# Optimization experiments

Hardware: AMD Instinct MI355X
Metric: run time of the kernel (lower is better)

The kernel has to match this reference:

```python
import jax, jax.numpy as jnp
import numpy as np

N_NODES = 20000
N_EDGES = 160000
DIM = 64          # node embedding dim
SUB = 16          # sub_dim
NB = 5            # n_bonds_type
RB = 8            # radial basis size (FeNNol default)
CUTOFF = 5.0
NLAYERS = 3
HID = 64          # conv_hidden
NSPEC = 86        # species onehot size
XI_SHAPE = RB * SUB * NB   # 640
FC_IN = XI_SHAPE + SUB     # 656
LOG2 = float(np.log(2.0))


def ssp(x):
    # shifted softplus activation
    return jax.nn.softplus(x) - jnp.asarray(LOG2, x.dtype)


def radial_bessel(r):
    # sine Bessel radial basis on [0, cutoff]; r: [E] -> [E, RB]
    n = jnp.arange(1, RB + 1, dtype=r.dtype)
    x = r[:, None]
    return jnp.sqrt(jnp.asarray(2.0 / CUTOFF, r.dtype)) * jnp.sin(n * jnp.pi * x / CUTOFF) / x


def setup_inputs() -> dict:
    key = jax.random.key(0)
    ks = jax.random.split(key, 16)
    inp = {}
    inp['species'] = jax.random.randint(ks[0], (N_NODES,), 1, NSPEC, dtype=jnp.int32)
    inp['edge_src'] = jnp.sort(jax.random.randint(ks[1], (N_EDGES,), 0, N_NODES, dtype=jnp.int32))
    inp['edge_dst'] = jax.random.randint(ks[2], (N_EDGES,), 0, N_NODES, dtype=jnp.int32)
    # distances kept away from 0 to keep 1/r finite
    inp['distances'] = jax.random.uniform(ks[3], (N_EDGES,), jnp.float32, 0.5, CUTOFF)
    inp['switch'] = jax.random.uniform(ks[4], (N_EDGES,), jnp.float32)
    inp['bond_order'] = jax.random.uniform(ks[5], (N_EDGES, NB), jnp.float32)
    s = lambda fan: 1.0 / np.sqrt(fan)
    inp['W_species'] = jax.random.normal(ks[6], (NSPEC, DIM), jnp.float32) * s(NSPEC)
    inp['Wl'] = jax.random.normal(ks[7], (NLAYERS, DIM, 2 * SUB), jnp.float32) * s(DIM)
    inp['bl'] = jnp.zeros((NLAYERS, 2 * SUB), jnp.float32)
    inp['fcW1'] = jax.random.normal(ks[8], (NLAYERS, FC_IN, HID), jnp.float32) * s(FC_IN)
    inp['fcb1'] = jnp.zeros((NLAYERS, HID), jnp.float32)
    inp['fcW2'] = jax.random.normal(ks[9], (NLAYERS, HID, HID), jnp.float32) * s(HID)
    inp['fcb2'] = jnp.zeros((NLAYERS, HID), jnp.float32)
    inp['fcW3'] = jax.random.normal(ks[10], (NLAYERS, HID, DIM), jnp.float32) * s(HID)
    inp['fcb3'] = jnp.zeros((NLAYERS, DIM), jnp.float32)
    return inp


def reference(species, edge_src, edge_dst, distances, switch, bond_order,
              W_species, Wl, bl, fcW1, fcb1, fcW2, fcb2, fcW3, fcb3):
    # onehot(species) @ W (no bias) == embedding gather
    xi = W_species[species]                      # [N, DIM]
    rb = radial_bessel(distances)                # [E, RB]
    sw = switch[:, None]                         # [E, 1]
    for l in range(NLAYERS):
        h = xi @ Wl[l] + bl[l]                   # [N, 2*SUB]
        si, mi = h[:, :SUB], h[:, SUB:]
        # per-edge outer product: [E, RB, SUB, NB] -> [E, RB*SUB*NB]
        xi_j = (rb[:, :, None, None]
                * mi[edge_dst][:, None, :, None]
                * bond_order[:, None, None, :]).reshape(N_EDGES, XI_SHAPE)
        dxi = jax.ops.segment_sum(xi_j * sw, edge_src, num_segments=N_NODES)  # [N, 640]
        dxi = jnp.concatenate([dxi, si], axis=-1)                             # [N, 656]
        dxi = ssp(dxi @ fcW1[l] + fcb1[l])
        dxi = ssp(dxi @ fcW2[l] + fcb2[l])
        dxi = dxi @ fcW3[l] + fcb3[l]            # last FC layer linear
        xi = xi + dxi
    return xi
```

## Files before the change

kernel.cpp:

```cpp
#include <hip/hip_runtime.h>
#include <math.h>

#define N_NODES 20000
#define N_EDGES 160000
#define EPAD    160256
#define NGROUPS (EPAD / 8)
#define GSTRIDE 320
#define NTILES  1250

#define PI_F 3.14159265358979323846f
#define LN2_F 0.69314718055994530942f

#define W1PK 43008
#define W23PK 4096
#define WPK_LAYER 51200
#define WLPK_LAYER 2048
#define XROW 680
#define CAP 312
#define NFILL_MAX 272

#define NW_EDGE 626
#define NW_XI   625
#define NW_PACK 616
#define NW_ROW  79
#define NW_TOTAL (NW_EDGE + NW_XI + NW_PACK + NW_ROW)

typedef short short8v __attribute__((ext_vector_type(8)));
typedef float f32x4 __attribute__((ext_vector_type(4)));
typedef unsigned short u16;
typedef unsigned long long ull;

__device__ __forceinline__ float sspf(float x) {
    return fmaxf(x, 0.0f) + log1pf(expf(-fabsf(x))) - LN2_F;
}
__device__ __forceinline__ u16 f2bf(float f) {
    unsigned int u = __float_as_uint(f);
    return (u16)((u + 0x7fffu + ((u >> 16) & 1u)) >> 16);
}
__device__ __forceinline__ unsigned int pk2(float a, float b) {
    return (unsigned int)f2bf(a) | ((unsigned int)f2bf(b) << 16);
}
__device__ __forceinline__ ull mge(int t) {
    t = t < 0 ? 0 : (t > 4 ? 4 : t);
    return t == 4 ? 0ULL : (~0ULL << (t * 16));
}

__device__ void edge_wt_work(int blk, const float* __restrict__ dist,
                             const float* __restrict__ sw,
                             const float* __restrict__ bo,
                             u16* __restrict__ WTg, char* smem)
{
    u16 (*tr)[264] = reinterpret_cast<u16(*)[264]>(smem);
    int tid = threadIdx.x;
    int e = blk * 256 + tid;

    if (e < N_EDGES) {
        float r = dist[e];
        float c = sqrtf(0.4f) / r * sw[e];
        float th = PI_F * r * 0.2f;
        float s1, c1;
        __sincosf(th, &s1, &c1);
        float k2c = 2.0f * c1;
        float rbv[8];
        rbv[0] = s1;
        float sp = 0.0f, sc = s1;
        #pragma unroll
        for (int n = 1; n < 8; ++n) {
            float sn = k2c * sc - sp;
            rbv[n] = sn;
            sp = sc; sc = sn;
        }
        #pragma unroll
        for (int n = 0; n < 8; ++n) rbv[n] *= c;
        float bov[5];
        #pragma unroll
        for (int b = 0; b < 5; ++b) bov[b] = bo[(size_t)e * 5 + b];
        #pragma unroll
        for (int n = 0; n < 8; ++n)
            #pragma unroll
            for (int b = 0; b < 5; ++b)
                tr[n * 5 + b][tid] = f2bf(rbv[n] * bov[b]);
    } else {
        #pragma unroll
        for (int j = 0; j < 40; ++j) tr[j][tid] = 0;
    }
    __syncthreads();

    #pragma unroll
    for (int i = 0; i < 5; ++i) {
        int r = i * 8 + (tid & 7);
        int gl = tid >> 3;
        uint4 v = *reinterpret_cast<const uint4*>(&tr[r][gl * 8]);
        *reinterpret_cast<uint4*>(
            WTg + ((size_t)(blk * 32 + gl) * GSTRIDE + r * 8)) = v;
    }
}

__device__ void row_start_work(int blk, const int* __restrict__ src,
                               int* __restrict__ row)
{
    int i = blk * 256 + threadIdx.x;
    if (i > N_NODES) return;
    int lo = 0, hi = N_EDGES;
    while (lo < hi) {
        int mid = (lo + hi) >> 1;
        if (src[mid] < i) lo = mid + 1; else hi = mid;
    }
    row[i] = lo;
}

__device__ void pack_w_work(int blk, const float* __restrict__ fcW1,
                            const float* __restrict__ fcW2,
                            const float* __restrict__ fcW3,
                            const float* __restrict__ Wl,
                            u16* __restrict__ Wpk,
                            u16* __restrict__ Wlpk)
{
    int idx = blk * 256 + threadIdx.x;
    if (idx >= 3 * WPK_LAYER + 2 * WLPK_LAYER) return;
    if (idx >= 3 * WPK_LAYER) {
        int r2 = idx - 3 * WPK_LAYER;
        int layer2 = r2 >> 11;
        int e = r2 & 2047;
        int j = e & 7, lane = (e >> 3) & 63;
        int rest = e >> 9;
        int ks = rest >> 1, cf = rest & 1;
        int k = ks * 32 + (lane >> 4) * 8 + j;
        int col = cf * 16 + (lane & 15);
        Wlpk[(size_t)layer2 * WLPK_LAYER + e] =
            f2bf(Wl[(size_t)(layer2 + 1) * 64 * 32 + (size_t)k * 32 + col]);
        return;
    }
    int layer = idx / WPK_LAYER;
    int r = idx - layer * WPK_LAYER;
    float val = 0.0f;
    if (r < W1PK) {
        int e = r;
        int j = e & 7, lane = (e >> 3) & 63, c16 = (e >> 9) & 3, ks = e >> 11;
        int k = ks * 32 + (lane >> 4) * 8 + j;
        int colm = c16 * 16 + (lane & 15);
        if (k < 640) {
            int nbv = k >> 4, ss = k & 15;
            int nn = nbv / 5, bb = nbv - nn * 5;
            val = fcW1[(size_t)layer * 656 * 64 + (size_t)(nn * 80 + ss * 5 + bb) * 64 + colm];
        } else if (k < 656) {
            val = fcW1[(size_t)layer * 656 * 64 + (size_t)k * 64 + colm];
        }
    } else {
        bool is2 = (r < W1PK + W23PK);
        const float* W = is2 ? fcW2 : fcW3;
        int e = is2 ? (r - W1PK) : (r - W1PK - W23PK);
        int j = e & 7, lane = (e >> 3) & 63, c16 = (e >> 9) & 3, ks = e >> 11;
        int k = ks * 32 + (lane >> 4) * 8 + j;
        int colm = c16 * 16 + (lane & 15);
        val = W[(size_t)layer * 64 * 64 + (size_t)k * 64 + colm];
    }
    Wpk[(size_t)layer * WPK_LAYER + r] = f2bf(val);
}

__device__ void xi_init_h_work(int blk, const int* __restrict__ species,
                               const float* __restrict__ Wsp,
                               const float* __restrict__ Wl0,
                               const float* __restrict__ bl0,
                               float* __restrict__ xi,
                               float* __restrict__ h, char* smem)
{
    float* xs = reinterpret_cast<float*>(smem);
    float* ws = reinterpret_cast<float*>(smem + 8192);
    int tid = threadIdx.x;
    int nb = blk * 32;

    #pragma unroll
    for (int i = 0; i < 2; ++i) {
        int idx = tid + i * 256;
        int node = idx >> 4, c4 = idx & 15;
        int sp = species[nb + node];
        float4 v = reinterpret_cast<const float4*>(Wsp + (size_t)sp * 64)[c4];
        reinterpret_cast<float4*>(xs)[idx] = v;
        reinterpret_cast<float4*>(xi)[(size_t)(nb + node) * 16 + c4] = v;
    }
    {
        const float4* wsrc = reinterpret_cast<const float4*>(Wl0);
        float4* wd = reinterpret_cast<float4*>(ws);
        #pragma unroll
        for (int i = 0; i < 2; ++i) wd[tid + i * 256] = wsrc[tid + i * 256];
    }
    __syncthreads();

    int c4g = tid & 7;
    int nrow = tid >> 3;
    float4 acc = *reinterpret_cast<const float4*>(bl0 + c4g * 4);
    const float* xr = xs + nrow * 64;
    #pragma unroll 8
    for (int j = 0; j < 64; ++j) {
        float xv = xr[j];
        float4 wv = *reinterpret_cast<const float4*>(ws + j * 32 + c4g * 4);
        acc.x = fmaf(xv, wv.x, acc.x);
        acc.y = fmaf(xv, wv.y, acc.y);
        acc.z = fmaf(xv, wv.z, acc.z);
        acc.w = fmaf(xv, wv.w, acc.w);
    }
    *reinterpret_cast<float4*>(h + (size_t)(nb + nrow) * 32 + c4g * 4) = acc;
}

__global__ __launch_bounds__(256) void setup_kernel(
    const float* __restrict__ dist, const float* __restrict__ sw,
    const float* __restrict__ bo, u16* __restrict__ WTg,
    const int* __restrict__ species, const float* __restrict__ Wsp,
    const float* __restrict__ Wl, const float* __restrict__ bl0,
    float* __restrict__ xi, float* __restrict__ h0,
    const float* __restrict__ fcW1, const float* __restrict__ fcW2,
    const float* __restrict__ fcW3, u16* __restrict__ Wpk,
    u16* __restrict__ Wlpk,
    const int* __restrict__ esrc, int* __restrict__ rowp)
{
    __shared__ __align__(16) char smem[21760];
    int wk = blockIdx.x;
    if (wk < NW_EDGE)
        edge_wt_work(wk, dist, sw, bo, WTg, smem);
    else if (wk < NW_EDGE + NW_XI)
        xi_init_h_work(wk - NW_EDGE, species, Wsp, Wl, bl0, xi, h0, smem);
    else if (wk < NW_EDGE + NW_XI + NW_PACK)
        pack_w_work(wk - NW_EDGE - NW_XI, fcW1, fcW2, fcW3, Wl, Wpk, Wlpk);
    else
        row_start_work(wk - NW_EDGE - NW_XI - NW_PACK, esrc, rowp);
}

__global__ __launch_bounds__(256) void agg_fc_fused(
    const u16* __restrict__ WTg,
    const int* __restrict__ row,
    const int* __restrict__ dst,
    const float* __restrict__ h_in,
    float* __restrict__ h_out,
    const u16* __restrict__ Wpk,
    const float* __restrict__ b1,
    const float* __restrict__ b2,
    const float* __restrict__ b3,
    const u16* __restrict__ Wlpk_l,
    const float* __restrict__ bl_next,
    int do_h,
    float* __restrict__ xi)
{
    __shared__ __align__(16) char smem[21760 + 16 * CAP * 2];
    u16 (*Xs)[XROW] = reinterpret_cast<u16(*)[XROW]>(smem);
    u16* mi  = reinterpret_cast<u16*>(smem + 21760);
    u16* Y1  = reinterpret_cast<u16*>(smem + 21760);
    u16* Y2  = reinterpret_cast<u16*>(smem + 21760 + 2304);
    float* Yo = reinterpret_cast<float*>(smem + 21760 + 4608);
    u16* Xnb  = reinterpret_cast<u16*>(smem + 8192);

    int tid = threadIdx.x;
    int wv = tid >> 6;
    int lane = tid & 63;
    int s = lane & 15;
    int kg = lane >> 4;
    int n0 = blockIdx.x * 16;
    int base = n0 + (wv << 2);

    int E0 = row[n0];
    int E1 = row[n0 + 16];
    int G0 = E0 & ~7;
    int nfill = E1 - G0;
    if (nfill > NFILL_MAX) nfill = NFILL_MAX;

    {
        int t = kg;
        u16* xr = &Xs[(wv << 2) + t][0];
        xr[640 + s] = f2bf(h_in[(size_t)(base + t) * 32 + s]);
        xr[656 + s] = 0;
    }

    for (int i = tid; i < nfill; i += 256) {
        int d = dst[G0 + i];
        const float4* hp = reinterpret_cast<const float4*>(h_in + (size_t)d * 32 + 16);
        float4 v0 = hp[0], v1 = hp[1], v2 = hp[2], v3 = hp[3];
        u16* col = mi + i;
        col[0 * CAP]  = f2bf(v0.x); col[1 * CAP]  = f2bf(v0.y);
        col[2 * CAP]  = f2bf(v0.z); col[3 * CAP]  = f2bf(v0.w);
        col[4 * CAP]  = f2bf(v1.x); col[5 * CAP]  = f2bf(v1.y);
        col[6 * CAP]  = f2bf(v1.z); col[7 * CAP]  = f2bf(v1.w);
        col[8 * CAP]  = f2bf(v2.x); col[9 * CAP]  = f2bf(v2.y);
        col[10 * CAP] = f2bf(v2.z); col[11 * CAP] = f2bf(v2.w);
        col[12 * CAP] = f2bf(v3.x); col[13 * CAP] = f2bf(v3.y);
        col[14 * CAP] = f2bf(v3.z); col[15 * CAP] = f2bf(v3.w);
    }
    __syncthreads();

    for (int t = 0; t < 4; ++t) {
        int node = base + t;
        int e0 = row[node], e1 = row[node + 1];
        int e0a = e0 & ~7;
        int L0 = e0a - G0;
        int nks = (e1 - e0a + 31) >> 5;

        f32x4 c0 = {0.f, 0.f, 0.f, 0.f};
        f32x4 c1 = {0.f, 0.f, 0.f, 0.f};
        f32x4 c2 = {0.f, 0.f, 0.f, 0.f};

        for (int kc = 0; kc < nks; ++kc) {
            int ebg = e0a + kc * 32 + kg * 8;
            int ebl = L0 + kc * 32 + kg * 8;
            uint4 bu = *reinterpret_cast<const uint4*>(mi + s * CAP + ebl);
            {
                int lo = e0 - ebg, hi = e1 - ebg;
                ull vA = mge(lo) & ~mge(hi);
                ull vB = mge(lo - 4) & ~mge(hi - 4);
                ull* bp = reinterpret_cast<ull*>(&bu);
                bp[0] &= vA;
                bp[1] &= vB;
            }
            short8v bfrag = *reinterpret_cast<short8v*>(&bu);
            const u16* gp = WTg + (size_t)(ebg >> 3) * GSTRIDE + (size_t)s * 8;
            short8v a0 = *reinterpret_cast<const short8v*>(gp);
            short8v a1 = *reinterpret_cast<const short8v*>(gp + 128);
            short8v a2 = {0, 0, 0, 0, 0, 0, 0, 0};
            if (s < 8)
                a2 = *reinterpret_cast<const short8v*>(gp + 256);
            c0 = __builtin_amdgcn_mfma_f32_16x16x32_bf16(a0, bfrag, c0, 0, 0, 0);
            c1 = __builtin_amdgcn_mfma_f32_16x16x32_bf16(a1, bfrag, c1, 0, 0, 0);
            c2 = __builtin_amdgcn_mfma_f32_16x16x32_bf16(a2, bfrag, c2, 0, 0, 0);
        }

        u16* xr = &Xs[(wv << 2) + t][0];
        #pragma unroll
        for (int q = 0; q < 4; ++q) {
            xr[(kg * 4 + q) * 16 + s]      = f2bf(c0[q]);
            xr[(16 + kg * 4 + q) * 16 + s] = f2bf(c1[q]);
        }
        if (kg < 2) {
            #pragma unroll
            for (int q = 0; q < 4; ++q)
                xr[(32 + kg * 4 + q) * 16 + s] = f2bf(c2[q]);
        }
    }
    __syncthreads();

    int w = wv;
    int lrow = lane & 15;
    int lk = lane >> 4;
    int col = w * 16 + lrow;

    const u16* Wpk1 = Wpk;
    const u16* Wpk2 = Wpk + W1PK;
    const u16* Wpk3 = Wpk + W1PK + W23PK;

    f32x4 acc;
    {
        float bv = b1[col];
        acc[0] = bv; acc[1] = bv; acc[2] = bv; acc[3] = bv;
    }
    const u16* wp = Wpk1 + ((size_t)w * 64 + lane) * 8;
    #pragma unroll
    for (int ks = 0; ks < 21; ++ks) {
        short8v a = *reinterpret_cast<const short8v*>(&Xs[lrow][ks * 32 + lk * 8]);
        short8v b = *reinterpret_cast<const short8v*>(wp + (size_t)ks * 2048);
        acc = __builtin_amdgcn_mfma_f32_16x16x32_bf16(a, b, acc, 0, 0, 0);
    }
    __syncthreads();
    #pragma unroll
    for (int q = 0; q < 4; ++q)
        Y1[(lk * 4 + q) * 72 + col] = f2bf(sspf(acc[q]));
    __syncthreads();

    {
        float bv = b2[col];
        acc[0] = bv; acc[1] = bv; acc[2] = bv; acc[3] = bv;
    }
    #pragma unroll
    for (int ks = 0; ks < 2; ++ks) {
        short8v a = *reinterpret_cast<const short8v*>(&Y1[lrow * 72 + ks * 32 + lk * 8]);
        short8v b = *reinterpret_cast<const short8v*>(Wpk2 + ((size_t)(ks * 4 + w) * 64 + lane) * 8);
        acc = __builtin_amdgcn_mfma_f32_16x16x32_bf16(a, b, acc, 0, 0, 0);
    }
    __syncthreads();
    #pragma unroll
    for (int q = 0; q < 4; ++q)
        Y2[(lk * 4 + q) * 72 + col] = f2bf(sspf(acc[q]));
    __syncthreads();

    {
        float bv = b3[col];
        acc[0] = bv; acc[1] = bv; acc[2] = bv; acc[3] = bv;
    }
    #pragma unroll
    for (int ks = 0; ks < 2; ++ks) {
        short8v a = *reinterpret_cast<const short8v*>(&Y2[lrow * 72 + ks * 32 + lk * 8]);
        short8v b = *reinterpret_cast<const short8v*>(Wpk3 + ((size_t)(ks * 4 + w) * 64 + lane) * 8);
        acc = __builtin_amdgcn_mfma_f32_16x16x32_bf16(a, b, acc, 0, 0, 0);
    }
    #pragma unroll
    for (int q = 0; q < 4; ++q)
        Yo[(lk * 4 + q) * 68 + col] = acc[q];
    __syncthreads();

    {
        int rr = tid >> 4;
        int cc = tid & 15;
        float4 dv = *reinterpret_cast<const float4*>(Yo + rr * 68 + cc * 4);
        float4* xpn = reinterpret_cast<float4*>(xi + (size_t)(n0 + rr) * 64 + cc * 4);
        float4 o = *xpn;
        o.x += dv.x; o.y += dv.y; o.z += dv.z; o.w += dv.w;
        *xpn = o;
        if (do_h) {
            unsigned int* xb = reinterpret_cast<unsigned int*>(Xnb + rr * 64 + cc * 4);
            xb[0] = pk2(o.x, o.y);
            xb[1] = pk2(o.z, o.w);
        }
    }

    if (do_h) {
        __syncthreads();
        if (wv < 2) {
            int cf = wv;
            f32x4 hacc;
            {
                float bv = bl_next[cf * 16 + lrow];
                hacc[0] = bv; hacc[1] = bv; hacc[2] = bv; hacc[3] = bv;
            }
            #pragma unroll
            for (int ks = 0; ks < 2; ++ks) {
                short8v a = *reinterpret_cast<const short8v*>(
                    Xnb + lrow * 64 + ks * 32 + lk * 8);
                short8v b = *reinterpret_cast<const short8v*>(
                    Wlpk_l + ((size_t)(ks * 2 + cf) * 64 + lane) * 8);
                hacc = __builtin_amdgcn_mfma_f32_16x16x32_bf16(a, b, hacc, 0, 0, 0);
            }
            #pragma unroll
            for (int q = 0; q < 4; ++q)
                h_out[(size_t)(n0 + lk * 4 + q) * 32 + cf * 16 + lrow] = hacc[q];
        }
    }
}

extern "C" void kernel_launch(void* const* d_in, const int* in_sizes, int n_in,
                              void* d_out, int out_size, void* d_ws, size_t ws_size,
                              hipStream_t stream) {
    const int*   species = (const int*)d_in[0];
    const int*   esrc    = (const int*)d_in[1];
    const int*   edst    = (const int*)d_in[2];
    const float* dist    = (const float*)d_in[3];
    const float* sw      = (const float*)d_in[4];
    const float* bo      = (const float*)d_in[5];
    const float* Wsp     = (const float*)d_in[6];
    const float* Wl      = (const float*)d_in[7];
    const float* bl      = (const float*)d_in[8];
    const float* fcW1    = (const float*)d_in[9];
    const float* fcb1    = (const float*)d_in[10];
    const float* fcW2    = (const float*)d_in[11];
    const float* fcb2    = (const float*)d_in[12];
    const float* fcW3    = (const float*)d_in[13];
    const float* fcb3    = (const float*)d_in[14];
    float* xi = (float*)d_out;

    char* ws = (char*)d_ws;
    u16*   WTg  = (u16*)ws;
    int*   rowp = (int*)(ws + 12820480);
    float* h0   = (float*)(ws + 12900608);
    float* h1   = (float*)(ws + 15460608);
    u16*   Wpk  = (u16*)(ws + 18020608);
    u16*   Wlpk = (u16*)(ws + 18327808);

    hipLaunchKernelGGL(setup_kernel, dim3(NW_TOTAL), dim3(256), 0, stream,
                       dist, sw, bo, WTg,
                       species, Wsp, Wl, bl, xi, h0,
                       fcW1, fcW2, fcW3, Wpk, Wlpk,
                       esrc, rowp);

    float* hbuf[2] = {h0, h1};
    for (int l = 0; l < 3; ++l) {
        int do_h = (l < 2) ? 1 : 0;
        hipLaunchKernelGGL(agg_fc_fused, dim3(NTILES), dim3(256), 0, stream,
                           WTg, rowp, edst,
                           hbuf[l & 1], hbuf[(l + 1) & 1],
                           Wpk + (size_t)l * WPK_LAYER,
                           fcb1 + (size_t)l * 64, fcb2 + (size_t)l * 64,
                           fcb3 + (size_t)l * 64,
                           Wlpk + (size_t)(do_h ? l : 0) * WLPK_LAYER,
                           bl + (size_t)(l + (do_h ? 1 : 0)) * 32,
                           do_h, xi);
    }
}
```

Measured before the change: 84.11 us.

## Recompute edge radial/bond weights in LDS inside fused aggregation kernel

Measured after the change: 84.15 us. No clear change (+0.1%).

```diff
diff --git a/kernel.cpp b/kernel.cpp
--- a/kernel.cpp
+++ b/kernel.cpp
@@ -3,9 +3,6 @@
 
 #define N_NODES 20000
 #define N_EDGES 160000
-#define EPAD    160256
-#define NGROUPS (EPAD / 8)
-#define GSTRIDE 320
 #define NTILES  1250
 
 #define PI_F 3.14159265358979323846f
@@ -16,14 +13,15 @@
 #define WPK_LAYER 51200
 #define WLPK_LAYER 2048
 #define XROW 680
-#define CAP 312
-#define NFILL_MAX 272
-
-#define NW_EDGE 626
+#define CAP 272
+#define NFILL_MAX 232
+#define WT_SLOTS 272
+#define GSTRIDE 320
+
 #define NW_XI   625
 #define NW_PACK 616
 #define NW_ROW  79
-#define NW_TOTAL (NW_EDGE + NW_XI + NW_PACK + NW_ROW)
+#define NW_TOTAL (NW_XI + NW_PACK + NW_ROW)
 
 typedef short short8v __attribute__((ext_vector_type(8)));
 typedef float f32x4 __attribute__((ext_vector_type(4)));
@@ -45,56 +43,6 @@
     return t == 4 ? 0ULL : (~0ULL << (t * 16));
 }
 
-__device__ void edge_wt_work(int blk, const float* __restrict__ dist,
-                             const float* __restrict__ sw,
-                             const float* __restrict__ bo,
-                             u16* __restrict__ WTg, char* smem)
-{
-    u16 (*tr)[264] = reinterpret_cast<u16(*)[264]>(smem);
-    int tid = threadIdx.x;
-    int e = blk * 256 + tid;
-
-    if (e < N_EDGES) {
-        float r = dist[e];
-        float c = sqrtf(0.4f) / r * sw[e];
-        float th = PI_F * r * 0.2f;
-        float s1, c1;
-        __sincosf(th, &s1, &c1);
-        float k2c = 2.0f * c1;
-        float rbv[8];
-        rbv[0] = s1;
-        float sp = 0.0f, sc = s1;
-        #pragma unroll
-        for (int n = 1; n < 8; ++n) {
-            float sn = k2c * sc - sp;
-            rbv[n] = sn;
-            sp = sc; sc = sn;
-        }
-        #pragma unroll
-        for (int n = 0; n < 8; ++n) rbv[n] *= c;
-        float bov[5];
-        #pragma unroll
-        for (int b = 0; b < 5; ++b) bov[b] = bo[(size_t)e * 5 + b];
-        #pragma unroll
-        for (int n = 0; n < 8; ++n)
-            #pragma unroll
-            for (int b = 0; b < 5; ++b)
-                tr[n * 5 + b][tid] = f2bf(rbv[n] * bov[b]);
-    } else {
-        #pragma unroll
-        for (int j = 0; j < 40; ++j) tr[j][tid] = 0;
-    }
-    __syncthreads();
-
-    #pragma unroll
-    for (int i = 0; i < 5; ++i) {
-        int r = i * 8 + (tid & 7);
-        int gl = tid >> 3;
-        uint4 v = *reinterpret_cast<const uint4*>(&tr[r][gl * 8]);
-        *reinterpret_cast<uint4*>(
-            WTg + ((size_t)(blk * 32 + gl) * GSTRIDE + r * 8)) = v;
-    }
-}
 
 __device__ void row_start_work(int blk, const int* __restrict__ src,
                                int* __restrict__ row)
@@ -204,8 +152,6 @@
 }
 
 __global__ __launch_bounds__(256) void setup_kernel(
-    const float* __restrict__ dist, const float* __restrict__ sw,
-    const float* __restrict__ bo, u16* __restrict__ WTg,
     const int* __restrict__ species, const float* __restrict__ Wsp,
     const float* __restrict__ Wl, const float* __restrict__ bl0,
     float* __restrict__ xi, float* __restrict__ h0,
@@ -214,20 +160,20 @@
     u16* __restrict__ Wlpk,
     const int* __restrict__ esrc, int* __restrict__ rowp)
 {
-    __shared__ __align__(16) char smem[21760];
+    __shared__ __align__(16) char smem[16384];
     int wk = blockIdx.x;
-    if (wk < NW_EDGE)
-        edge_wt_work(wk, dist, sw, bo, WTg, smem);
-    else if (wk < NW_EDGE + NW_XI)
-        xi_init_h_work(wk - NW_EDGE, species, Wsp, Wl, bl0, xi, h0, smem);
-    else if (wk < NW_EDGE + NW_XI + NW_PACK)
-        pack_w_work(wk - NW_EDGE - NW_XI, fcW1, fcW2, fcW3, Wl, Wpk, Wlpk);
+    if (wk < NW_XI)
+        xi_init_h_work(wk, species, Wsp, Wl, bl0, xi, h0, smem);
+    else if (wk < NW_XI + NW_PACK)
+        pack_w_work(wk - NW_XI, fcW1, fcW2, fcW3, Wl, Wpk, Wlpk);
     else
-        row_start_work(wk - NW_EDGE - NW_XI - NW_PACK, esrc, rowp);
+        row_start_work(wk - NW_XI - NW_PACK, esrc, rowp);
 }
 
 __global__ __launch_bounds__(256) void agg_fc_fused(
-    const u16* __restrict__ WTg,
+    const float* __restrict__ dist,
+    const float* __restrict__ sw,
+    const float* __restrict__ bo,
     const int* __restrict__ row,
     const int* __restrict__ dst,
     const float* __restrict__ h_in,
@@ -241,9 +187,10 @@
     int do_h,
     float* __restrict__ xi)
 {
-    __shared__ __align__(16) char smem[21760 + 16 * CAP * 2];
+    __shared__ __align__(16) char smem[52224];
     u16 (*Xs)[XROW] = reinterpret_cast<u16(*)[XROW]>(smem);
-    u16* mi  = reinterpret_cast<u16*>(smem + 21760);
+    u16* wt  = reinterpret_cast<u16*>(smem + 21760);
+    u16* mi  = reinterpret_cast<u16*>(smem + 43520);
     u16* Y1  = reinterpret_cast<u16*>(smem + 21760);
     u16* Y2  = reinterpret_cast<u16*>(smem + 21760 + 2304);
     float* Yo = reinterpret_cast<float*>(smem + 21760 + 4608);
@@ -268,6 +215,41 @@
         u16* xr = &Xs[(wv << 2) + t][0];
         xr[640 + s] = f2bf(h_in[(size_t)(base + t) * 32 + s]);
         xr[656 + s] = 0;
+    }
+
+    for (int i = tid; i < WT_SLOTS; i += 256) {
+        int e = G0 + i;
+        u16* wcol = wt + (i >> 3) * GSTRIDE + (i & 7);
+        if (i < nfill && e < N_EDGES) {
+            float r = dist[e];
+            float c = sqrtf(0.4f) / r * sw[e];
+            float th = PI_F * r * 0.2f;
+            float s1, c1v;
+            __sincosf(th, &s1, &c1v);
+            float k2c = 2.0f * c1v;
+            float rbv[8];
+            rbv[0] = s1;
+            float sp = 0.0f, sc = s1;
+            #pragma unroll
+            for (int n = 1; n < 8; ++n) {
+                float sn = k2c * sc - sp;
+                rbv[n] = sn;
+                sp = sc; sc = sn;
+            }
+            #pragma unroll
+            for (int n = 0; n < 8; ++n) rbv[n] *= c;
+            float bov[5];
+            #pragma unroll
+            for (int b = 0; b < 5; ++b) bov[b] = bo[(size_t)e * 5 + b];
+            #pragma unroll
+            for (int n = 0; n < 8; ++n)
+                #pragma unroll
+                for (int b = 0; b < 5; ++b)
+                    wcol[(n * 5 + b) * 8] = f2bf(rbv[n] * bov[b]);
+        } else {
+            #pragma unroll
+            for (int r2 = 0; r2 < 40; ++r2) wcol[r2 * 8] = 0;
+        }
     }
 
     for (int i = tid; i < nfill; i += 256) {
@@ -292,6 +274,8 @@
         int e0a = e0 & ~7;
         int L0 = e0a - G0;
         int nks = (e1 - e0a + 31) >> 5;
+        int maxks = (264 - L0) >> 5;
+        if (nks > maxks) nks = maxks;
 
         f32x4 c0 = {0.f, 0.f, 0.f, 0.f};
         f32x4 c1 = {0.f, 0.f, 0.f, 0.f};
@@ -310,7 +294,7 @@
                 bp[1] &= vB;
             }
             short8v bfrag = *reinterpret_cast<short8v*>(&bu);
-            const u16* gp = WTg + (size_t)(ebg >> 3) * GSTRIDE + (size_t)s * 8;
+            const u16* gp = wt + (ebl >> 3) * GSTRIDE + s * 8;
             short8v a0 = *reinterpret_cast<const short8v*>(gp);
             short8v a1 = *reinterpret_cast<const short8v*>(gp + 128);
             short8v a2 = {0, 0, 0, 0, 0, 0, 0, 0};
@@ -453,15 +437,13 @@
     float* xi = (float*)d_out;
 
     char* ws = (char*)d_ws;
-    u16*   WTg  = (u16*)ws;
-    int*   rowp = (int*)(ws + 12820480);
-    float* h0   = (float*)(ws + 12900608);
-    float* h1   = (float*)(ws + 15460608);
-    u16*   Wpk  = (u16*)(ws + 18020608);
-    u16*   Wlpk = (u16*)(ws + 18327808);
+    int*   rowp = (int*)ws;
+    float* h0   = (float*)(ws + 80128);
+    float* h1   = (float*)(ws + 2640128);
+    u16*   Wpk  = (u16*)(ws + 5200128);
+    u16*   Wlpk = (u16*)(ws + 5507328);
 
     hipLaunchKernelGGL(setup_kernel, dim3(NW_TOTAL), dim3(256), 0, stream,
-                       dist, sw, bo, WTg,
                        species, Wsp, Wl, bl, xi, h0,
                        fcW1, fcW2, fcW3, Wpk, Wlpk,
                        esrc, rowp);
@@ -470,7 +452,7 @@
     for (int l = 0; l < 3; ++l) {
         int do_h = (l < 2) ? 1 : 0;
         hipLaunchKernelGGL(agg_fc_fused, dim3(NTILES), dim3(256), 0, stream,
-                           WTg, rowp, edst,
+                           dist, sw, bo, rowp, edst,
                            hbuf[l & 1], hbuf[(l + 1) & 1],
                            Wpk + (size_t)l * WPK_LAYER,
                            fcb1 + (size_t)l * 64, fcb2 + (size_t)l * 64,
```

## Process two 16-node tiles per block with double-buffered neighbour gather

Applied to the files above, without the earlier changes.

New measurement: 92.65 us. 10.2% more time.

```diff
diff --git a/kernel.cpp b/kernel.cpp
--- a/kernel.cpp
+++ b/kernel.cpp
@@ -6,7 +6,7 @@
 #define EPAD    160256
 #define NGROUPS (EPAD / 8)
 #define GSTRIDE 320
-#define NTILES  1250
+#define NBLK    625
 
 #define PI_F 3.14159265358979323846f
 #define LN2_F 0.69314718055994530942f
@@ -16,8 +16,8 @@
 #define WPK_LAYER 51200
 #define WLPK_LAYER 2048
 #define XROW 680
-#define CAP 312
-#define NFILL_MAX 272
+#define CAP 280
+#define NFILL_MAX 232
 
 #define NW_EDGE 626
 #define NW_XI   625
@@ -241,195 +241,219 @@
     int do_h,
     float* __restrict__ xi)
 {
-    __shared__ __align__(16) char smem[21760 + 16 * CAP * 2];
+    __shared__ __align__(16) char smem[39680];
     u16 (*Xs)[XROW] = reinterpret_cast<u16(*)[XROW]>(smem);
-    u16* mi  = reinterpret_cast<u16*>(smem + 21760);
-    u16* Y1  = reinterpret_cast<u16*>(smem + 21760);
-    u16* Y2  = reinterpret_cast<u16*>(smem + 21760 + 2304);
-    float* Yo = reinterpret_cast<float*>(smem + 21760 + 4608);
-    u16* Xnb  = reinterpret_cast<u16*>(smem + 8192);
+    u16* miA = reinterpret_cast<u16*>(smem + 21760);
+    u16* miB = reinterpret_cast<u16*>(smem + 30720);
+    u16* Xnb = reinterpret_cast<u16*>(smem + 8192);
 
     int tid = threadIdx.x;
     int wv = tid >> 6;
     int lane = tid & 63;
     int s = lane & 15;
     int kg = lane >> 4;
-    int n0 = blockIdx.x * 16;
-    int base = n0 + (wv << 2);
-
-    int E0 = row[n0];
-    int E1 = row[n0 + 16];
-    int G0 = E0 & ~7;
-    int nfill = E1 - G0;
-    if (nfill > NFILL_MAX) nfill = NFILL_MAX;
-
+    int lrow = lane & 15;
+    int lk = lane >> 4;
+    int col = wv * 16 + lrow;
+    int rr = tid >> 4;
+    int cc = tid & 15;
+
+    const u16* Wpk1 = Wpk;
+    const u16* Wpk2 = Wpk + W1PK;
+    const u16* Wpk3 = Wpk + W1PK + W23PK;
+
+    int n0a = blockIdx.x * 32;
+    int n0b = n0a + 16;
+
+    int E0a = row[n0a], E1a = row[n0a + 16];
+    int G0a = E0a & ~7;
+    int nfa = E1a - G0a; if (nfa > NFILL_MAX) nfa = NFILL_MAX;
+    int E0b = row[n0b], E1b = row[n0b + 16];
+    int G0b = E0b & ~7;
+    int nfb = E1b - G0b; if (nfb > NFILL_MAX) nfb = NFILL_MAX;
+
+#define GATHER(G0x, nfx, mix)                                                  \
+    for (int i = tid; i < (nfx); i += 256) {                                   \
+        int d = dst[(G0x) + i];                                                \
+        const float4* hp = reinterpret_cast<const float4*>(h_in + (size_t)d * 32 + 16); \
+        float4 v0 = hp[0], v1 = hp[1], v2 = hp[2], v3 = hp[3];                 \
+        u16* colp = (mix) + i;                                                 \
+        colp[0 * CAP]  = f2bf(v0.x); colp[1 * CAP]  = f2bf(v0.y);              \
+        colp[2 * CAP]  = f2bf(v0.z); colp[3 * CAP]  = f2bf(v0.w);              \
+        colp[4 * CAP]  = f2bf(v1.x); colp[5 * CAP]  = f2bf(v1.y);              \
+        colp[6 * CAP]  = f2bf(v1.z); colp[7 * CAP]  = f2bf(v1.w);              \
+        colp[8 * CAP]  = f2bf(v2.x); colp[9 * CAP]  = f2bf(v2.y);              \
+        colp[10 * CAP] = f2bf(v2.z); colp[11 * CAP] = f2bf(v2.w);              \
+        colp[12 * CAP] = f2bf(v3.x); colp[13 * CAP] = f2bf(v3.y);              \
+        colp[14 * CAP] = f2bf(v3.z); colp[15 * CAP] = f2bf(v3.w);              \
+    }
+
+#define PHASEA(n0x, G0x, mix)                                                  \
+    for (int t = 0; t < 4; ++t) {                                              \
+        int node = (n0x) + (wv << 2) + t;                                      \
+        int e0 = row[node], e1 = row[node + 1];                                \
+        int e0a = e0 & ~7;                                                     \
+        int L0 = e0a - (G0x);                                                  \
+        int nks = (e1 - e0a + 31) >> 5;                                        \
+        int maxks = (272 - L0) >> 5;                                           \
+        if (nks > maxks) nks = maxks;                                          \
+        f32x4 c0 = {0.f, 0.f, 0.f, 0.f};                                       \
+        f32x4 c1 = {0.f, 0.f, 0.f, 0.f};                                       \
+        f32x4 c2 = {0.f, 0.f, 0.f, 0.f};                                       \
+        for (int kc = 0; kc < nks; ++kc) {                                     \
+            int ebg = e0a + kc * 32 + kg * 8;                                  \
+            int ebl = L0 + kc * 32 + kg * 8;                                   \
+            uint4 bu = *reinterpret_cast<const uint4*>((mix) + s * CAP + ebl); \
+            {                                                                  \
+                int lo = e0 - ebg, hi = e1 - ebg;                              \
+                ull vA = mge(lo) & ~mge(hi);                                   \
+                ull vB = mge(lo - 4) & ~mge(hi - 4);                           \
+                ull* bp = reinterpret_cast<ull*>(&bu);                         \
+                bp[0] &= vA;                                                   \
+                bp[1] &= vB;                                                   \
+            }                                                                  \
+            short8v bfrag = *reinterpret_cast<short8v*>(&bu);                  \
+            const u16* gp = WTg + (size_t)(ebg >> 3) * GSTRIDE + (size_t)s * 8;\
+            short8v a0 = *reinterpret_cast<const short8v*>(gp);                \
+            short8v a1 = *reinterpret_cast<const short8v*>(gp + 128);          \
+            short8v a2 = {0, 0, 0, 0, 0, 0, 0, 0};                             \
+            if (s < 8)                                                         \
+                a2 = *reinterpret_cast<const short8v*>(gp + 256);              \
+            c0 = __builtin_amdgcn_mfma_f32_16x16x32_bf16(a0, bfrag, c0, 0, 0, 0); \
+            c1 = __builtin_amdgcn_mfma_f32_16x16x32_bf16(a1, bfrag, c1, 0, 0, 0); \
+            c2 = __builtin_amdgcn_mfma_f32_16x16x32_bf16(a2, bfrag, c2, 0, 0, 0); \
+        }                                                                      \
+        u16* xr = &Xs[(wv << 2) + t][0];                                       \
+        _Pragma("unroll")                                                      \
+        for (int q = 0; q < 4; ++q) {                                          \
+            xr[(kg * 4 + q) * 16 + s]      = f2bf(c0[q]);                      \
+            xr[(16 + kg * 4 + q) * 16 + s] = f2bf(c1[q]);                      \
+        }                                                                      \
+        if (kg < 2) {                                                          \
+            _Pragma("unroll")                                                  \
+            for (int q = 0; q < 4; ++q)                                        \
+                xr[(32 + kg * 4 + q) * 16 + s] = f2bf(c2[q]);                  \
+        }                                                                      \
+    }
+
+#define FC_AND_EPILOGUE(n0x, YREG)                                             \
+    {                                                                          \
+        u16* Y1 = (YREG);                                                      \
+        u16* Y2 = (YREG) + 1152;                        \
+        float* Yo = reinterpret_cast<float*>((YREG) + 2304);   \
+        f32x4 acc;                                                             \
+        {                                                                      \
+            float bv = b1[col];                                                \
+            acc[0] = bv; acc[1] = bv; acc[2] = bv; acc[3] = bv;                \
+        }                                                                      \
+        const u16* wp = Wpk1 + ((size_t)wv * 64 + lane) * 8;                   \
+        _Pragma("unroll")                                                      \
+        for (int ks = 0; ks < 21; ++ks) {                                      \
+            short8v a = *reinterpret_cast<const short8v*>(&Xs[lrow][ks * 32 + lk * 8]); \
+            short8v b = *reinterpret_cast<const short8v*>(wp + (size_t)ks * 2048); \
+            acc = __builtin_amdgcn_mfma_f32_16x16x32_bf16(a, b, acc, 0, 0, 0); \
+        }                                                                      \
+        _Pragma("unroll")                                                      \
+        for (int q = 0; q < 4; ++q)                                            \
+            Y1[(lk * 4 + q) * 72 + col] = f2bf(sspf(acc[q]));                  \
+        __syncthreads();                                                       \
+        {                                                                      \
+            float bv = b2[col];                                                \
+            acc[0] = bv; acc[1] = bv; acc[2] = bv; acc[3] = bv;                \
+        }                                                                      \
+        _Pragma("unroll")                                                      \
+        for (int ks = 0; ks < 2; ++ks) {                                       \
+            short8v a = *reinterpret_cast<const short8v*>(&Y1[lrow * 72 + ks * 32 + lk * 8]); \
+            short8v b = *reinterpret_cast<const short8v*>(Wpk2 + ((size_t)(ks * 4 + wv) * 64 + lane) * 8); \
+            acc = __builtin_amdgcn_mfma_f32_16x16x32_bf16(a, b, acc, 0, 0, 0); \
+        }                                                                      \
+        __syncthreads();                                                       \
+        _Pragma("unroll")                                                      \
+        for (int q = 0; q < 4; ++q)                                            \
+            Y2[(lk * 4 + q) * 72 + col] = f2bf(sspf(acc[q]));                  \
+        __syncthreads();                                                       \
+        {                                                                      \
+            float bv = b3[col];                                                \
+            acc[0] = bv; acc[1] = bv; acc[2] = bv; acc[3] = bv;                \
+        }                                                                      \
+        _Pragma("unroll")                                                      \
+        for (int ks = 0; ks < 2; ++ks) {                                       \
+            short8v a = *reinterpret_cast<const short8v*>(&Y2[lrow * 72 + ks * 32 + lk * 8]); \
+            short8v b = *reinterpret_cast<const short8v*>(Wpk3 + ((size_t)(ks * 4 + wv) * 64 + lane) * 8); \
+            acc = __builtin_amdgcn_mfma_f32_16x16x32_bf16(a, b, acc, 0, 0, 0); \
+        }                                                                      \
+        _Pragma("unroll")                                                      \
+        for (int q = 0; q < 4; ++q)                                            \
+            Yo[(lk * 4 + q) * 68 + col] = acc[q];                              \
+        __syncthreads();                                                       \
+        {                                                                      \
+            float4 dv = *reinterpret_cast<const float4*>(Yo + rr * 68 + cc * 4); \
+            float4* xpn = reinterpret_cast<float4*>(xi + (size_t)((n0x) + rr) * 64 + cc * 4); \
+            float4 o = *xpn;                                                   \
+            o.x += dv.x; o.y += dv.y; o.z += dv.z; o.w += dv.w;                \
+            *xpn = o;                                                          \
+            if (do_h) {                                                        \
+                unsigned int* xb = reinterpret_cast<unsigned int*>(Xnb + rr * 64 + cc * 4); \
+                xb[0] = pk2(o.x, o.y);                                         \
+                xb[1] = pk2(o.z, o.w);                                         \
+            }                                                                  \
+        }                                                                      \
+        if (do_h) {                                                            \
+            __syncthreads();                                                   \
+            if (wv < 2) {                                                      \
+                int cf = wv;                                                   \
+                f32x4 hacc;                                                    \
+                {                                                              \
+                    float bv = bl_next[cf * 16 + lrow];                        \
+                    hacc[0] = bv; hacc[1] = bv; hacc[2] = bv; hacc[3] = bv;    \
+                }                                                              \
+                _Pragma("unroll")                                              \
+                for (int ks = 0; ks < 2; ++ks) {                               \
+                    short8v a = *reinterpret_cast<const short8v*>(             \
+                        Xnb + lrow * 64 + ks * 32 + lk * 8);                   \
+                    short8v b = *reinterpret_cast<const short8v*>(             \
+                        Wlpk_l + ((size_t)(ks * 2 + cf) * 64 + lane) * 8);     \
+                    hacc = __builtin_amdgcn_mfma_f32_16x16x32_bf16(a, b, hacc, 0, 0, 0); \
+                }                                                              \
+                _Pragma("unroll")                                              \
+                for (int q = 0; q < 4; ++q)                                    \
+                    h_out[(size_t)((n0x) + lk * 4 + q) * 32 + cf * 16 + lrow] = hacc[q]; \
+            }                                                                  \
+        }                                                                      \
+    }
+
+    float siT1;
     {
         int t = kg;
         u16* xr = &Xs[(wv << 2) + t][0];
-        xr[640 + s] = f2bf(h_in[(size_t)(base + t) * 32 + s]);
+        xr[640 + s] = f2bf(h_in[(size_t)(n0a + (wv << 2) + t) * 32 + s]);
         xr[656 + s] = 0;
-    }
-
-    for (int i = tid; i < nfill; i += 256) {
-        int d = dst[G0 + i];
-        const float4* hp = reinterpret_cast<const float4*>(h_in + (size_t)d * 32 + 16);
-        float4 v0 = hp[0], v1 = hp[1], v2 = hp[2], v3 = hp[3];
-        u16* col = mi + i;
-        col[0 * CAP]  = f2bf(v0.x); col[1 * CAP]  = f2bf(v0.y);
-        col[2 * CAP]  = f2bf(v0.z); col[3 * CAP]  = f2bf(v0.w);
-        col[4 * CAP]  = f2bf(v1.x); col[5 * CAP]  = f2bf(v1.y);
-        col[6 * CAP]  = f2bf(v1.z); col[7 * CAP]  = f2bf(v1.w);
-        col[8 * CAP]  = f2bf(v2.x); col[9 * CAP]  = f2bf(v2.y);
-        col[10 * CAP] = f2bf(v2.z); col[11 * CAP] = f2bf(v2.w);
-        col[12 * CAP] = f2bf(v3.x); col[13 * CAP] = f2bf(v3.y);
-        col[14 * CAP] = f2bf(v3.z); col[15 * CAP] = f2bf(v3.w);
-    }
+        siT1 = h_in[(size_t)(n0b + (wv << 2) + t) * 32 + s];
+    }
+    GATHER(G0a, nfa, miA)
     __syncthreads();
 
-    for (int t = 0; t < 4; ++t) {
-        int node = base + t;
-        int e0 = row[node], e1 = row[node + 1];
-        int e0a = e0 & ~7;
-        int L0 = e0a - G0;
-        int nks = (e1 - e0a + 31) >> 5;
-
-        f32x4 c0 = {0.f, 0.f, 0.f, 0.f};
-        f32x4 c1 = {0.f, 0.f, 0.f, 0.f};
-        f32x4 c2 = {0.f, 0.f, 0.f, 0.f};
-
-        for (int kc = 0; kc < nks; ++kc) {
-            int ebg = e0a + kc * 32 + kg * 8;
-            int ebl = L0 + kc * 32 + kg * 8;
-            uint4 bu = *reinterpret_cast<const uint4*>(mi + s * CAP + ebl);
-            {
-                int lo = e0 - ebg, hi = e1 - ebg;
-                ull vA = mge(lo) & ~mge(hi);
-                ull vB = mge(lo - 4) & ~mge(hi - 4);
-                ull* bp = reinterpret_cast<ull*>(&bu);
-                bp[0] &= vA;
-                bp[1] &= vB;
-            }
-            short8v bfrag = *reinterpret_cast<short8v*>(&bu);
-            const u16* gp = WTg + (size_t)(ebg >> 3) * GSTRIDE + (size_t)s * 8;
-            short8v a0 = *reinterpret_cast<const short8v*>(gp);
-            short8v a1 = *reinterpret_cast<const short8v*>(gp + 128);
-            short8v a2 = {0, 0, 0, 0, 0, 0, 0, 0};
-            if (s < 8)
-                a2 = *reinterpret_cast<const short8v*>(gp + 256);
-            c0 = __builtin_amdgcn_mfma_f32_16x16x32_bf16(a0, bfrag, c0, 0, 0, 0);
-            c1 = __builtin_amdgcn_mfma_f32_16x16x32_bf16(a1, bfrag, c1, 0, 0, 0);
-            c2 = __builtin_amdgcn_mfma_f32_16x16x32_bf16(a2, bfrag, c2, 0, 0, 0);
-        }
-
+    GATHER(G0b, nfb, miB)
+    PHASEA(n0a, G0a, miA)
+    __syncthreads();
+
+    FC_AND_EPILOGUE(n0a, miA)
+    __syncthreads();
+
+    {
+        int t = kg;
         u16* xr = &Xs[(wv << 2) + t][0];
-        #pragma unroll
-        for (int q = 0; q < 4; ++q) {
-            xr[(kg * 4 + q) * 16 + s]      = f2bf(c0[q]);
-            xr[(16 + kg * 4 + q) * 16 + s] = f2bf(c1[q]);
-        }
-        if (kg < 2) {
-            #pragma unroll
-            for (int q = 0; q < 4; ++q)
-                xr[(32 + kg * 4 + q) * 16 + s] = f2bf(c2[q]);
-        }
-    }
+        xr[640 + s] = f2bf(siT1);
+        xr[656 + s] = 0;
+    }
+    PHASEA(n0b, G0b, miB)
     __syncthreads();
 
-    int w = wv;
-    int lrow = lane & 15;
-    int lk = lane >> 4;
-    int col = w * 16 + lrow;
-
-    const u16* Wpk1 = Wpk;
-    const u16* Wpk2 = Wpk + W1PK;
-    const u16* Wpk3 = Wpk + W1PK + W23PK;
-
-    f32x4 acc;
-    {
-        float bv = b1[col];
-        acc[0] = bv; acc[1] = bv; acc[2] = bv; acc[3] = bv;
-    }
-    const u16* wp = Wpk1 + ((size_t)w * 64 + lane) * 8;
-    #pragma unroll
-    for (int ks = 0; ks < 21; ++ks) {
-        short8v a = *reinterpret_cast<const short8v*>(&Xs[lrow][ks * 32 + lk * 8]);
-        short8v b = *reinterpret_cast<const short8v*>(wp + (size_t)ks * 2048);
-        acc = __builtin_amdgcn_mfma_f32_16x16x32_bf16(a, b, acc, 0, 0, 0);
-    }
-    __syncthreads();
-    #pragma unroll
-    for (int q = 0; q < 4; ++q)
-        Y1[(lk * 4 + q) * 72 + col] = f2bf(sspf(acc[q]));
-    __syncthreads();
-
-    {
-        float bv = b2[col];
-        acc[0] = bv; acc[1] = bv; acc[2] = bv; acc[3] = bv;
-    }
-    #pragma unroll
-    for (int ks = 0; ks < 2; ++ks) {
-        short8v a = *reinterpret_cast<const short8v*>(&Y1[lrow * 72 + ks * 32 + lk * 8]);
-        short8v b = *reinterpret_cast<const short8v*>(Wpk2 + ((size_t)(ks * 4 + w) * 64 + lane) * 8);
-        acc = __builtin_amdgcn_mfma_f32_16x16x32_bf16(a, b, acc, 0, 0, 0);
-    }
-    __syncthreads();
-    #pragma unroll
-    for (int q = 0; q < 4; ++q)
-        Y2[(lk * 4 + q) * 72 + col] = f2bf(sspf(acc[q]));
-    __syncthreads();
-
-    {
-        float bv = b3[col];
-        acc[0] = bv; acc[1] = bv; acc[2] = bv; acc[3] = bv;
-    }
-    #pragma unroll
-    for (int ks = 0; ks < 2; ++ks) {
-        short8v a = *reinterpret_cast<const short8v*>(&Y2[lrow * 72 + ks * 32 + lk * 8]);
-        short8v b = *reinterpret_cast<const short8v*>(Wpk3 + ((size_t)(ks * 4 + w) * 64 + lane) * 8);
-        acc = __builtin_amdgcn_mfma_f32_16x16x32_bf16(a, b, acc, 0, 0, 0);
-    }
-    #pragma unroll
-    for (int q = 0; q < 4; ++q)
-        Yo[(lk * 4 + q) * 68 + col] = acc[q];
-    __syncthreads();
-
-    {
-        int rr = tid >> 4;
-        int cc = tid & 15;
-        float4 dv = *reinterpret_cast<const float4*>(Yo + rr * 68 + cc * 4);
-        float4* xpn = reinterpret_cast<float4*>(xi + (size_t)(n0 + rr) * 64 + cc * 4);
-        float4 o = *xpn;
-        o.x += dv.x; o.y += dv.y; o.z += dv.z; o.w += dv.w;
-        *xpn = o;
-        if (do_h) {
-            unsigned int* xb = reinterpret_cast<unsigned int*>(Xnb + rr * 64 + cc * 4);
-            xb[0] = pk2(o.x, o.y);
-            xb[1] = pk2(o.z, o.w);
-        }
-    }
-
-    if (do_h) {
-        __syncthreads();
-        if (wv < 2) {
-            int cf = wv;
-            f32x4 hacc;
-            {
-                float bv = bl_next[cf * 16 + lrow];
-                hacc[0] = bv; hacc[1] = bv; hacc[2] = bv; hacc[3] = bv;
-            }
-            #pragma unroll
-            for (int ks = 0; ks < 2; ++ks) {
-                short8v a = *reinterpret_cast<const short8v*>(
-                    Xnb + lrow * 64 + ks * 32 + lk * 8);
-                short8v b = *reinterpret_cast<const short8v*>(
-                    Wlpk_l + ((size_t)(ks * 2 + cf) * 64 + lane) * 8);
-                hacc = __builtin_amdgcn_mfma_f32_16x16x32_bf16(a, b, hacc, 0, 0, 0);
-            }
-            #pragma unroll
-            for (int q = 0; q < 4; ++q)
-                h_out[(size_t)(n0 + lk * 4 + q) * 32 + cf * 16 + lrow] = hacc[q];
-        }
-    }
+    FC_AND_EPILOGUE(n0b, miB)
+
+#undef GATHER
+#undef PHASEA
+#undef FC_AND_EPILOGUE
 }
 
 extern "C" void kernel_launch(void* const* d_in, const int* in_sizes, int n_in,
@@ -469,7 +493,7 @@
     float* hbuf[2] = {h0, h1};
     for (int l = 0; l < 3; ++l) {
         int do_h = (l < 2) ? 1 : 0;
-        hipLaunchKernelGGL(agg_fc_fused, dim3(NTILES), dim3(256), 0, stream,
+        hipLaunchKernelGGL(agg_fc_fused, dim3(NBLK), dim3(256), 0, stream,
                            WTg, rowp, edst,
                            hbuf[l & 1], hbuf[(l + 1) & 1],
                            Wpk + (size_t)l * WPK_LAYER,
```
